# Kernel optimization log

Measured on AMD Instinct MI355X. Metric: run time of the kernel, lower is better.

The kernel has to match this reference:

```python
import jax, jax.numpy as jnp
import numpy as np

K = 16          # hardcoded in generate_graph (self.k = 16, KNNGraph(k=16))
TEMP = 0.5      # gumbel-softmax temperature
GRID = 0.5      # grid_size init arg
EPS = 1e-20


def mlp2(h, W1, b1, W2, b2):
    # tgnn.models.MLP(num_layers=2): Linear -> BN(eval init = identity) -> ReLU -> Linear
    return jax.nn.relu(h @ W1 + b1) @ W2 + b2


def pairwise_sqdist(a, b):
    d2 = (a * a).sum(-1)[:, None] + (b * b).sum(-1)[None, :] - 2.0 * (a @ b.T)
    return jnp.maximum(d2, 0.0)


def setup_inputs() -> dict:
    key = jax.random.key(0)
    ks = jax.random.split(key, 16)
    N, Cin, Cout = 8192, 64, 128

    def lin(k, fi, fo):
        return jax.random.normal(k, (fi, fo), jnp.float32) / np.sqrt(fi)

    return dict(
        x=jax.random.normal(ks[0], (N, Cin), jnp.float32),
        pos=jax.random.uniform(ks[1], (N, 3), jnp.float32) * 10.0,
        # generate_graph.MLP: Cin -> Cin -> 10
        Wg1=lin(ks[2], Cin, Cin), bg1=jnp.zeros((Cin,), jnp.float32),
        Wg2=lin(ks[3], Cin, 10), bg2=jnp.zeros((10,), jnp.float32),
        # PointTransformerConv linears (bias=False in PyG)
        Wlin=lin(ks[4], Cin, Cout),
        Wsrc=lin(ks[5], Cin, Cout),
        Wdst=lin(ks[6], Cin, Cout),
        # pos_nn MLP: 3 -> Cout -> Cout
        Wp1=lin(ks[7], 3, Cout), bp1=jnp.zeros((Cout,), jnp.float32),
        Wp2=lin(ks[8], Cout, Cout), bp2=jnp.zeros((Cout,), jnp.float32),
        # attn_nn MLP: Cout -> Cout -> Cout
        Wa1=lin(ks[9], Cout, Cout), ba1=jnp.zeros((Cout,), jnp.float32),
        Wa2=lin(ks[10], Cout, Cout), ba2=jnp.zeros((Cout,), jnp.float32),
        # down: Linear -> BN(eval identity) -> ReLU
        Wd=lin(ks[11], Cout, Cout), bd=jnp.zeros((Cout,), jnp.float32),
    )


def forward_core(x, pos, Wg1, bg1, Wg2, bg2, Wlin, Wsrc, Wdst,
                 Wp1, bp1, Wp2, bp2, Wa1, ba1, Wa2, ba2, Wd, bd):
    N = x.shape[0]
    rk = jax.random.split(jax.random.key(42), 2)

    # ---- KNNGraph(k=16) on pos: sources = k nearest neighbors, targets = centers ----
    d2p = pairwise_sqdist(pos, pos)
    d2p = d2p.at[jnp.arange(N), jnp.arange(N)].set(jnp.inf)
    _, knn_idx = jax.lax.top_k(-d2p, K)              # [N, K]
    tgt = jnp.repeat(jnp.arange(N), K)               # [N*K]
    knn_src = knn_idx.reshape(-1)

    # ---- gumbel-softmax soft edges on learned embedding ----
    emb = mlp2(x, Wg1, bg1, Wg2, bg2)                # [N, 10]
    emb = emb + jax.random.uniform(rk[0], emb.shape, emb.dtype) * 0.001
    d2e = pairwise_sqdist(emb, emb)                  # dist**2, [N, N]
    u = jax.random.uniform(rk[1], (N, N), jnp.float32)
    gumbel = -jnp.log(-jnp.log(u + EPS) + EPS)
    noisy = jnp.log(jnp.exp(-d2e) + EPS) + gumbel
    probs = jax.nn.softmax(noisy / TEMP, axis=0)     # softmax over dim 0, as in source
    top_v, top_i = jax.lax.top_k(probs, K)           # topk over last axis
    soft_src = top_i.reshape(-1)

    # combined edge_index = [soft edges ; knn edges]  (generate_graph cat order)
    src = jnp.concatenate([soft_src, knn_src])
    dst = jnp.concatenate([tgt, tgt])
    w = jnp.concatenate([top_v.reshape(-1), jnp.ones((N * K,), x.dtype)])

    # ---- PointTransformerConv (vector attention); soft edges weighted by gumbel probs ----
    a_src = (x @ Wsrc)[src]                          # [E, C]
    a_dst = (x @ Wdst)[dst]
    v_src = (x @ Wlin)[src]
    delta = mlp2(pos[dst] - pos[src], Wp1, bp1, Wp2, bp2)     # [E, C]
    logits = mlp2(a_dst - a_src + delta, Wa1, ba1, Wa2, ba2)  # [E, C]
    m = jax.ops.segment_max(logits, dst, num_segments=N)
    e = jnp.exp(logits - m[dst])
    s = jax.ops.segment_sum(e, dst, num_segments=N)
    attn = e / (s[dst] + 1e-16)                      # per-target softmax
    msg = attn * (v_src + delta) * w[:, None]
    h = jax.ops.segment_sum(msg, dst, num_segments=N)         # [N, C]

    # ---- down: Linear -> BN(eval, identity at init) -> ReLU ----
    h = jax.nn.relu(h @ Wd + bd)

    # ---- max_pool_neighbor_x (max over neighbors incl. self-loop) ----
    pooled = jax.ops.segment_max(h[src], dst, num_segments=N)
    h = jnp.maximum(h, pooled)

    # ---- GridSampling(GRID): mean-pool x and pos per voxel, padded to N clusters ----
    v = jnp.floor((pos - pos.min(axis=0)) / GRID).astype(jnp.int32)
    nv = v.max(axis=0) + 1
    vid = (v[:, 0] * nv[1] + v[:, 1]) * nv[2] + v[:, 2]
    _, inv = jnp.unique(vid, size=N, fill_value=-1, return_inverse=True)
    cnt = jax.ops.segment_sum(jnp.ones((N,), x.dtype), inv, num_segments=N)
    denom = jnp.maximum(cnt, 1.0)[:, None]
    x_out = jax.ops.segment_sum(h, inv, num_segments=N) / denom
    pos_out = jax.ops.segment_sum(pos, inv, num_segments=N) / denom
    return x_out, pos_out, cnt


def reference(x, pos, Wg1, bg1, Wg2, bg2, Wlin, Wsrc, Wdst,
              Wp1, bp1, Wp2, bp2, Wa1, ba1, Wa2, ba2, Wd, bd):
    return forward_core(x, pos, Wg1, bg1, Wg2, bg2, Wlin, Wsrc, Wdst,
                        Wp1, bp1, Wp2, bp2, Wa1, ba1, Wa2, ba2, Wd, bd)
```

## Files before the change

### kernel.cpp

```cpp
#include <hip/hip_runtime.h>
#include <stdint.h>


typedef unsigned int u32;
typedef float v2f __attribute__((ext_vector_type(2)));
typedef float f32x4 __attribute__((ext_vector_type(4)));
typedef short bf16x8 __attribute__((ext_vector_type(8)));

#define NN 8192
#define EPS20 1e-20f
#define QSCALE 489.0671f

__host__ __device__ static inline u32 bf16rne(float x){
  u32 b = __float_as_uint(x);
  return (b + 0x7fffu + ((b>>16)&1u)) >> 16;
}

__host__ __device__ static inline u32 rotl32(u32 v, int r){ return (v<<r)|(v>>(32-r)); }

__host__ __device__ static inline void tf2x32(u32 k0, u32 k1, u32 c0, u32 c1, u32& o0, u32& o1){
  u32 ks2 = k0 ^ k1 ^ 0x1BD11BDAu;
  u32 x0 = c0 + k0;
  u32 x1 = c1 + k1;
#define TFR(r) x0 += x1; x1 = rotl32(x1,(r)); x1 ^= x0;
  TFR(13) TFR(15) TFR(26) TFR(6)
  x0 += k1;  x1 += ks2 + 1u;
  TFR(17) TFR(29) TFR(16) TFR(24)
  x0 += ks2; x1 += k0 + 2u;
  TFR(13) TFR(15) TFR(26) TFR(6)
  x0 += k0;  x1 += k1 + 3u;
  TFR(17) TFR(29) TFR(16) TFR(24)
  x0 += k1;  x1 += ks2 + 4u;
  TFR(13) TFR(15) TFR(26) TFR(6)
  x0 += ks2; x1 += k0 + 5u;
#undef TFR
  o0 = x0; o1 = x1;
}

__device__ static inline u32 rbits(u32 k0, u32 k1, u32 idx){
  u32 o0,o1; tf2x32(k0,k1, 0u, idx, o0,o1);
  return o0 ^ o1;
}

__device__ static inline float u01(u32 b){
  return __uint_as_float((b>>9) | 0x3f800000u) - 1.0f;
}

__device__ static inline float gumbel_g(u32 ub){
  float u = u01(ub);
  float w = -__logf(u + EPS20);
  return -__logf(w + EPS20);
}

static constexpr size_t OFF_EMBF = 0;
static constexpr size_t OFF_SP   = OFF_EMBF + (size_t)8192*12*4;
static constexpr size_t OFF_PSUM = OFF_SP   + (size_t)8192*4;
static constexpr size_t OFF_SSRC = OFF_PSUM + (size_t)32*8192*4;
static constexpr size_t OFF_TOPV = OFF_SSRC + (size_t)8192*16*4;
static constexpr size_t OFF_KSRC = OFF_TOPV + (size_t)8192*16*4;
static constexpr size_t OFF_HIST = OFF_KSRC + (size_t)8192*16*4;
static constexpr size_t OFF_RANK = OFF_HIST + (size_t)8192*4;
static constexpr size_t OFF_UCNT = OFF_RANK + (size_t)8192*4;
static constexpr size_t OFF_VID  = OFF_UCNT + (size_t)8192*4;
static constexpr size_t OFF_META = OFF_VID  + (size_t)8192*4;
static constexpr size_t OFF_QKI  = OFF_META + 64;
static constexpr size_t OFF_CAND = OFF_QKI  + (size_t)8192*4;
static constexpr size_t OFF_POS4 = OFF_CAND + (size_t)8192*32*4;
static constexpr size_t OFF_WH   = (OFF_POS4 + (size_t)8192*16 + 255) & ~(size_t)255;
static constexpr size_t OFF_WL   = OFF_WH + (size_t)3*16384*2;
static constexpr size_t OFF_BIG  = (OFF_WL + (size_t)3*16384*2 + 255) & ~(size_t)255;
static constexpr size_t OFF_A    = OFF_BIG;
static constexpr size_t OFF_B    = OFF_A    + (size_t)8192*128*4;
static constexpr size_t OFF_V    = OFF_B    + (size_t)8192*128*4;
static constexpr size_t OFF_H    = OFF_V    + (size_t)8192*128*4;
static constexpr size_t OFF_HD   = OFF_H    + (size_t)8192*128*4;
static constexpr size_t OFF_Y    = OFF_HD   + (size_t)8192*128*4;
static constexpr size_t OFF_ACCX = OFF_Y    + (size_t)8192*128*4;
static constexpr size_t OFF_ACCP = OFF_ACCX + (size_t)8192*128*4;
static constexpr size_t OFF_ZQ   = OFF_BIG;
static constexpr size_t ZQ_BYTES = (size_t)NN*NN*2;


__global__ void k_init0(int* __restrict__ mi, int* __restrict__ mx){
  int t = threadIdx.x;
  if (t < 3){ mi[t] = 0x7f7fffff; mx[t] = 0; }
}

__global__ __launch_bounds__(128) void k_wprep(const float* __restrict__ Wp2,
    const float* __restrict__ Wa1, const float* __restrict__ Wa2,
    unsigned short* __restrict__ WH, unsigned short* __restrict__ WL){
  int m = blockIdx.x >> 7;
  int c = blockIdx.x & 127;
  int k = threadIdx.x;
  const float* Wm = (m==0) ? Wp2 : (m==1) ? Wa1 : Wa2;
  float x = Wm[k*128 + c];
  u32 hi = bf16rne(x);
  float lo = x - __uint_as_float(hi<<16);
  u32 lo16 = bf16rne(lo);
  size_t base = (size_t)m*16384 + (size_t)c*128 + k;
  WH[base] = (unsigned short)hi;
  WL[base] = (unsigned short)lo16;
}

__global__ __launch_bounds__(256) void k_min(const float* __restrict__ pos, int* __restrict__ mi){
  __shared__ int red[768];
  int t = threadIdx.x;
  int n = blockIdx.x*256 + t;
  red[t]     = __float_as_int(pos[n*3+0]);
  red[256+t] = __float_as_int(pos[n*3+1]);
  red[512+t] = __float_as_int(pos[n*3+2]);
  __syncthreads();
  for (int s=128; s>0; s>>=1){
    if (t < s){
      red[t]     = min(red[t],     red[t+s]);
      red[256+t] = min(red[256+t], red[256+t+s]);
      red[512+t] = min(red[512+t], red[512+t+s]);
    }
    __syncthreads();
  }
  if (t == 0){ atomicMin(&mi[0], red[0]); atomicMin(&mi[1], red[256]); atomicMin(&mi[2], red[512]); }
}

__global__ __launch_bounds__(256) void k_ext(const float* __restrict__ pos, const int* __restrict__ mi,
                                             int* __restrict__ mx){
  __shared__ int red[768];
  int t = threadIdx.x;
  int n = blockIdx.x*256 + t;
  float p0 = __int_as_float(mi[0]), p1 = __int_as_float(mi[1]), p2 = __int_as_float(mi[2]);
  red[t]     = (int)floorf((pos[n*3+0]-p0)*2.0f);
  red[256+t] = (int)floorf((pos[n*3+1]-p1)*2.0f);
  red[512+t] = (int)floorf((pos[n*3+2]-p2)*2.0f);
  __syncthreads();
  for (int s=128; s>0; s>>=1){
    if (t < s){
      red[t]     = max(red[t],     red[t+s]);
      red[256+t] = max(red[256+t], red[256+t+s]);
      red[512+t] = max(red[512+t], red[512+t+s]);
    }
    __syncthreads();
  }
  if (t == 0){ atomicMax(&mx[0], red[0]); atomicMax(&mx[1], red[256]); atomicMax(&mx[2], red[512]); }
}

__global__ __launch_bounds__(256) void k_vid(const float* __restrict__ pos,
                                             const int* __restrict__ mi, const int* __restrict__ mx,
                                             int* __restrict__ vid, int* __restrict__ hist,
                                             float4* __restrict__ pos4){
  int n = blockIdx.x*256 + threadIdx.x;
  float p0=pos[n*3], p1=pos[n*3+1], p2=pos[n*3+2];
  float4 p4; p4.x=p0; p4.y=p1; p4.z=p2; p4.w = p0*p0 + p1*p1 + p2*p2;
  pos4[n] = p4;
  float q0 = __int_as_float(mi[0]), q1 = __int_as_float(mi[1]), q2 = __int_as_float(mi[2]);
  int v0 = (int)floorf((p0-q0)*2.0f);
  int v1 = (int)floorf((p1-q1)*2.0f);
  int v2 = (int)floorf((p2-q2)*2.0f);
  int nv1 = mx[1]+1, nv2 = mx[2]+1;
  int id = (v0*nv1 + v1)*nv2 + v2;
  vid[n] = id;
  atomicAdd(&hist[id], 1);
}

__global__ __launch_bounds__(64) void k_emb(const float* __restrict__ x,
    const float* __restrict__ Wg1, const float* __restrict__ bg1,
    const float* __restrict__ Wg2, const float* __restrict__ bg2,
    u32 ka, u32 kb, float* __restrict__ embF){
  int i = blockIdx.x; int t = threadIdx.x;
  __shared__ float xs[64], hs[64], esq[10];
  xs[t] = x[i*64+t];
  __syncthreads();
  float a = bg1[t];
  for (int k=0; k<64; k++) a += xs[k]*Wg1[k*64+t];
  hs[t] = fmaxf(a, 0.0f);
  __syncthreads();
  if (t < 10){
    float e = bg2[t];
    for (int k=0; k<64; k++) e += hs[k]*Wg2[k*10+t];
    e += u01(rbits(ka, kb, (u32)(i*10+t))) * 0.001f;
    embF[i*12+t] = e;
    esq[t] = e*e;
  }
  __syncthreads();
  if (t == 0){
    float ssum = 0.0f;
    #pragma unroll
    for (int d=0; d<10; d++) ssum += esq[d];
    embF[i*12+10] = ssum;
    embF[i*12+11] = 0.0f;
  }
}

__global__ __launch_bounds__(64) void k_knn(const float4* __restrict__ pos4,
                                            int* __restrict__ knn_src){
  int i = blockIdx.x; int l = threadIdx.x;
  float4 pi = pos4[i];
  float lv[8]; int lj[8];
  #pragma unroll
  for (int s=0; s<8; s++){ lv[s]=1e30f; lj[s]=0x7fffffff; }
  for (int tt=0; tt<128; tt++){
    int j = l + 64*tt;
    float4 pj = pos4[j];
    float d = pi.w + pj.w - 2.0f*(pi.x*pj.x + pi.y*pj.y + pi.z*pj.z);
    d = fmaxf(d, 0.0f);
    if (j != i && d < lv[7]){
      lv[7]=d; lj[7]=j;
      #pragma unroll
      for (int s=7; s>0; s--){
        if (lv[s] < lv[s-1]){ float tv=lv[s]; lv[s]=lv[s-1]; lv[s-1]=tv; int tj=lj[s]; lj[s]=lj[s-1]; lj[s-1]=tj; }
      }
    }
  }
  for (int r=0; r<16; r++){
    float bv = lv[0]; int bj = lj[0];
    #pragma unroll
    for (int off=32; off>=1; off>>=1){
      float ov = __shfl_xor(bv, off);
      int   oj = __shfl_xor(bj, off);
      if (ov < bv || (ov == bv && oj < bj)){ bv = ov; bj = oj; }
    }
    if (l == 0) knn_src[i*16+r] = bj;
    if (lj[0] == bj){
      #pragma unroll
      for (int s=0; s<7; s++){ lv[s]=lv[s+1]; lj[s]=lj[s+1]; }
      lv[7]=1e30f; lj[7]=0x7fffffff;
    }
  }
}

template<bool STZ>
__global__ __launch_bounds__(256) void k_colstats(const float* __restrict__ embF,
                                                  u32 ka, u32 kb, float* __restrict__ psum,
                                                  unsigned short* __restrict__ zq){
  __shared__ float4 sE4[768];
  int t = threadIdx.x;
  int j = blockIdx.x*256 + t;
  int i0 = blockIdx.y*256;
  const float4* gF = (const float4*)embF;
  #pragma unroll
  for (int q=0; q<3; q++) sE4[t + 256*q] = gF[(size_t)i0*3 + t + 256*q];
  __syncthreads();
  float4 b0 = gF[j*3+0], b1 = gF[j*3+1], b2 = gF[j*3+2];
  float sej = b2.z;
  float s = 0.0f;
  unsigned short* zp = STZ ? (zq + ((size_t)i0<<13) + j) : nullptr;
  for (int r=0; r<256; r++){
    float4 a0 = sE4[r*3+0], a1 = sE4[r*3+1], a2 = sE4[r*3+2];
    float dot = a0.x*b0.x + a0.y*b0.y + a0.z*b0.z + a0.w*b0.w
              + a1.x*b1.x + a1.y*b1.y + a1.z*b1.z + a1.w*b1.w
              + a2.x*b2.x + a2.y*b2.y;
    float d2 = fmaxf(a2.z + sej - 2.0f*dot, 0.0f);
    float g = gumbel_g(rbits(ka, kb, (u32)(i0+r)*8192u + (u32)j));
    float z = 2.0f*(g - d2);
    s += __expf(z - 40.0f);
    if (STZ){
      float qf = (z + 100.0f)*QSCALE + 0.5f;
      qf = fminf(fmaxf(qf, 0.0f), 65535.0f);
      *zp = (unsigned short)qf;
      zp += NN;
    }
  }
  psum[blockIdx.y*NN + j] = s;
}

__global__ __launch_bounds__(256) void k_colfin(const float* __restrict__ psum, float* __restrict__ embF,
                                                int* __restrict__ qKi){
  int j = blockIdx.x*256 + threadIdx.x;
  float S = 0.0f;
  for (int c=0; c<32; c++) S += psum[c*NN + j];
  float K = 40.0f + __logf(S);
  embF[j*12+11] = K;
  qKi[j] = (int)((K + 100.0f)*QSCALE + 0.5f);
}

__global__ __launch_bounds__(64) void k_rowtopk(const float* __restrict__ embF,
    u32 ka, u32 kb, int* __restrict__ soft_src, float* __restrict__ top_v){
  int i = blockIdx.x; int l = threadIdx.x;
  const float4* gF = (const float4*)embF;
  float4 b0 = gF[i*3+0], b1 = gF[i*3+1], b2 = gF[i*3+2];
  float sei = b2.z;
  float lv[16]; int lj[16];
  #pragma unroll
  for (int s=0; s<16; s++){ lv[s]=-1e30f; lj[s]=0x7fffffff; }
  for (int tt=0; tt<128; tt++){
    int j = l + 64*tt;
    float4 a0 = gF[j*3+0], a1 = gF[j*3+1], a2 = gF[j*3+2];
    float dot = a0.x*b0.x + a0.y*b0.y + a0.z*b0.z + a0.w*b0.w
              + a1.x*b1.x + a1.y*b1.y + a1.z*b1.z + a1.w*b1.w
              + a2.x*b2.x + a2.y*b2.y;
    float d2 = fmaxf(a2.z + sei - 2.0f*dot, 0.0f);
    float g = gumbel_g(rbits(ka, kb, (u32)i*8192u + (u32)j));
    float z = 2.0f*(g - d2);
    float y = z - a2.w;
    if (y > lv[15]){
      lv[15]=y; lj[15]=j;
      #pragma unroll
      for (int s=15; s>0; s--){
        if (lv[s] > lv[s-1]){ float tv=lv[s]; lv[s]=lv[s-1]; lv[s-1]=tv; int tj=lj[s]; lj[s]=lj[s-1]; lj[s-1]=tj; }
      }
    }
  }
  for (int r=0; r<16; r++){
    float bv = lv[0]; int bj = lj[0];
    #pragma unroll
    for (int off=32; off>=1; off>>=1){
      float ov = __shfl_xor(bv, off);
      int   oj = __shfl_xor(bj, off);
      if (ov > bv || (ov == bv && oj < bj)){ bv = ov; bj = oj; }
    }
    if (l == 0){ soft_src[i*16+r] = bj; top_v[i*16+r] = __expf(bv); }
    if (lj[0] == bj){
      #pragma unroll
      for (int s=0; s<15; s++){ lv[s]=lv[s+1]; lj[s]=lj[s+1]; }
      lv[15]=-1e30f; lj[15]=0x7fffffff;
    }
  }
}

__global__ __launch_bounds__(64) void k_qtopk(const unsigned short* __restrict__ zq,
    const int* __restrict__ qKi, int* __restrict__ cand){
  int i = blockIdx.x; int l = threadIdx.x;
  const uint4* zrow = (const uint4*)(zq + ((size_t)i<<13));
  int lv[8]; int lj[8];
  #pragma unroll
  for (int s=0; s<8; s++){ lv[s]=-0x40000000; lj[s]=0x7fffffff; }
  for (int tt=0; tt<16; tt++){
    int blk = l + 64*tt;
    uint4 zv = zrow[blk];
    int jb = blk*8;
    const int4* qk4 = (const int4*)(qKi + jb);
    int4 ka4 = qk4[0], kb4 = qk4[1];
    u32 wv[4] = {zv.x, zv.y, zv.z, zv.w};
    int qk[8] = {ka4.x,ka4.y,ka4.z,ka4.w, kb4.x,kb4.y,kb4.z,kb4.w};
    #pragma unroll
    for (int c=0; c<8; c++){
      int qz = (int)((wv[c>>1] >> ((c&1)*16)) & 0xffffu);
      int qy = qz - qk[c];
      if (qy > lv[7]){
        lv[7]=qy; lj[7]=jb+c;
        #pragma unroll
        for (int s=7; s>0; s--){
          if (lv[s] > lv[s-1]){ int tv=lv[s]; lv[s]=lv[s-1]; lv[s-1]=tv; int tj=lj[s]; lj[s]=lj[s-1]; lj[s-1]=tj; }
        }
      }
    }
  }
  for (int r=0; r<32; r++){
    int bv = lv[0]; int bj = lj[0];
    #pragma unroll
    for (int off=32; off>=1; off>>=1){
      int ov = __shfl_xor(bv, off);
      int oj = __shfl_xor(bj, off);
      if (ov > bv || (ov == bv && oj < bj)){ bv = ov; bj = oj; }
    }
    if (l == 0) cand[i*32+r] = bj;
    if (lj[0] == bj){
      #pragma unroll
      for (int s=0; s<7; s++){ lv[s]=lv[s+1]; lj[s]=lj[s+1]; }
      lv[7]=-0x40000000; lj[7]=0x7fffffff;
    }
  }
}

__global__ __launch_bounds__(64) void k_rescore(const float* __restrict__ embF,
    const int* __restrict__ cand, u32 ka, u32 kb,
    int* __restrict__ soft_src, float* __restrict__ top_v){
  int i = blockIdx.x; int l = threadIdx.x;
  const float4* gF = (const float4*)embF;
  float4 b0 = gF[i*3+0], b1 = gF[i*3+1], b2 = gF[i*3+2];
  float sei = b2.z;
  float y = -1e30f; int jc = 0x7fffffff;
  if (l < 32){
    jc = cand[i*32+l];
    float4 a0 = gF[jc*3+0], a1 = gF[jc*3+1], a2 = gF[jc*3+2];
    float dot = a0.x*b0.x + a0.y*b0.y + a0.z*b0.z + a0.w*b0.w
              + a1.x*b1.x + a1.y*b1.y + a1.z*b1.z + a1.w*b1.w
              + a2.x*b2.x + a2.y*b2.y;
    float d2 = fmaxf(a2.z + sei - 2.0f*dot, 0.0f);
    float g = gumbel_g(rbits(ka, kb, (u32)i*8192u + (u32)jc));
    float z = 2.0f*(g - d2);
    y = z - a2.w;
  }
  for (int r=0; r<16; r++){
    float bv = y; int bj = jc;
    #pragma unroll
    for (int off=32; off>=1; off>>=1){
      float ov = __shfl_xor(bv, off);
      int   oj = __shfl_xor(bj, off);
      if (ov > bv || (ov == bv && oj < bj)){ bv = ov; bj = oj; }
    }
    if (l == 0){ soft_src[i*16+r] = bj; top_v[i*16+r] = __expf(bv); }
    if (jc == bj){ y = -1e30f; jc = 0x7fffffff; }
  }
}

__global__ __launch_bounds__(128) void k_xw(const float* __restrict__ x,
    const float* __restrict__ Wsrc, const float* __restrict__ Wdst, const float* __restrict__ Wlin,
    float* __restrict__ A, float* __restrict__ B, float* __restrict__ V){
  int g0 = blockIdx.x*8; int c = threadIdx.x;
  __shared__ float xs[8][64];
  for (int idx=c; idx<512; idx+=128) xs[idx>>6][idx&63] = x[(g0 + (idx>>6))*64 + (idx&63)];
  __syncthreads();
  float aA[8], aB[8], aV[8];
  #pragma unroll
  for (int g=0; g<8; g++){ aA[g]=0.0f; aB[g]=0.0f; aV[g]=0.0f; }
  for (int k=0; k<64; k++){
    float ws=Wsrc[k*128+c], wd=Wdst[k*128+c], wl=Wlin[k*128+c];
    #pragma unroll
    for (int g=0; g<8; g++){
      float xv = xs[g][k];
      aA[g] += xv*ws; aB[g] += xv*wd; aV[g] += xv*wl;
    }
  }
  #pragma unroll
  for (int g=0; g<8; g++){
    A[(g0+g)*128+c]=aA[g]; B[(g0+g)*128+c]=aB[g]; V[(g0+g)*128+c]=aV[g];
  }
}

#define MFMA3(WHP, WLP)                                                     \
  {                                                                         \
    _Pragma("unroll")                                                       \
    for (int s=0; s<4; s++){                                                \
      int kk = 32*s + 8*g;                                                  \
      bf16x8 a0h = *(const bf16x8*)(&ah[r0][kk]);                           \
      bf16x8 a1h = *(const bf16x8*)(&ah[16+r0][kk]);                        \
      bf16x8 a0l = *(const bf16x8*)(&al[r0][kk]);                           \
      bf16x8 a1l = *(const bf16x8*)(&al[16+r0][kk]);                        \
      const unsigned short* whp = (WHP) + (size_t)cn0*128 + kk;             \
      const unsigned short* wlp = (WLP) + (size_t)cn0*128 + kk;             \
      bf16x8 b0h = *(const bf16x8*)(whp);                                   \
      bf16x8 b1h = *(const bf16x8*)(whp + 2048);                            \
      bf16x8 b0l = *(const bf16x8*)(wlp);                                   \
      bf16x8 b1l = *(const bf16x8*)(wlp + 2048);                            \
      c00 = __builtin_amdgcn_mfma_f32_16x16x32_bf16(a0h,b0h,c00,0,0,0);     \
      c01 = __builtin_amdgcn_mfma_f32_16x16x32_bf16(a0h,b1h,c01,0,0,0);     \
      c10 = __builtin_amdgcn_mfma_f32_16x16x32_bf16(a1h,b0h,c10,0,0,0);     \
      c11 = __builtin_amdgcn_mfma_f32_16x16x32_bf16(a1h,b1h,c11,0,0,0);     \
      c00 = __builtin_amdgcn_mfma_f32_16x16x32_bf16(a0h,b0l,c00,0,0,0);     \
      c01 = __builtin_amdgcn_mfma_f32_16x16x32_bf16(a0h,b1l,c01,0,0,0);     \
      c10 = __builtin_amdgcn_mfma_f32_16x16x32_bf16(a1h,b0l,c10,0,0,0);     \
      c11 = __builtin_amdgcn_mfma_f32_16x16x32_bf16(a1h,b1l,c11,0,0,0);     \
      c00 = __builtin_amdgcn_mfma_f32_16x16x32_bf16(a0l,b0h,c00,0,0,0);     \
      c01 = __builtin_amdgcn_mfma_f32_16x16x32_bf16(a0l,b1h,c01,0,0,0);     \
      c10 = __builtin_amdgcn_mfma_f32_16x16x32_bf16(a1l,b0h,c10,0,0,0);     \
      c11 = __builtin_amdgcn_mfma_f32_16x16x32_bf16(a1l,b1h,c11,0,0,0);     \
    }                                                                       \
  }

__global__ __launch_bounds__(256) void k_edge(const float* __restrict__ pos,
    const int* __restrict__ soft_src, const float* __restrict__ top_v, const int* __restrict__ knn_src,
    const float* __restrict__ A, const float* __restrict__ B, const float* __restrict__ V,
    const float* __restrict__ Wp1, const float* __restrict__ bp1,
    const unsigned short* __restrict__ WH, const unsigned short* __restrict__ WL,
    const float* __restrict__ bp2, const float* __restrict__ ba1, const float* __restrict__ ba2,
    float* __restrict__ h){
  int i = blockIdx.x; int t = threadIdx.x;
  int l = t & 63; int w = t >> 6;
  int g = l >> 4; int r0 = l & 15;
  int cn0 = 32*w + r0;
  __shared__ __align__(16) unsigned short ah[32][136];
  __shared__ __align__(16) unsigned short al[32][136];
  __shared__ int   ssrc[32];
  __shared__ float sw[32];
  __shared__ float sdp[32][3];
  if (t < 32){
    int s; float wt;
    if (t < 16){ s = soft_src[i*16+t]; wt = top_v[i*16+t]; }
    else       { s = knn_src[i*16+(t-16)]; wt = 1.0f; }
    ssrc[t]=s; sw[t]=wt;
    sdp[t][0]=pos[i*3]-pos[s*3]; sdp[t][1]=pos[i*3+1]-pos[s*3+1]; sdp[t][2]=pos[i*3+2]-pos[s*3+2];
  }
  __syncthreads();
  {
    const float2* W1v = (const float2*)Wp1;
    float2 q0 = W1v[l], q1 = W1v[64+l], q2 = W1v[128+l];
    float2 bb = ((const float2*)bp1)[l];
    #pragma unroll
    for (int e=0; e<8; e++){
      int row = 8*w + e;
      float d0=sdp[row][0], d1=sdp[row][1], d2=sdp[row][2];
      float vx = fmaxf(d0*q0.x + d1*q1.x + d2*q2.x + bb.x, 0.0f);
      float vy = fmaxf(d0*q0.y + d1*q1.y + d2*q2.y + bb.y, 0.0f);
      u32 hx = bf16rne(vx), hy = bf16rne(vy);
      float lx = vx - __uint_as_float(hx<<16);
      float ly = vy - __uint_as_float(hy<<16);
      u32 lx16 = bf16rne(lx), ly16 = bf16rne(ly);
      *(u32*)(&ah[row][2*l]) = hx | (hy<<16);
      *(u32*)(&al[row][2*l]) = lx16 | (ly16<<16);
    }
  }
  __syncthreads();
  f32x4 c00={0,0,0,0}, c01={0,0,0,0}, c10={0,0,0,0}, c11={0,0,0,0};
  MFMA3(WH, WL);
  f32x4 dl00, dl01, dl10, dl11;
  {
    float bi0 = bp2[cn0], bi1 = bp2[cn0+16];
    #pragma unroll
    for (int r=0; r<4; r++){
      dl00[r]=c00[r]+bi0; dl01[r]=c01[r]+bi1;
      dl10[r]=c10[r]+bi0; dl11[r]=c11[r]+bi1;
    }
  }
  __syncthreads();
  int ssv[8];
  {
    float B0 = B[(size_t)i*128 + cn0];
    float B1 = B[(size_t)i*128 + cn0 + 16];
    #pragma unroll
    for (int m=0; m<2; m++){
      #pragma unroll
      for (int r=0; r<4; r++){
        int row = 16*m + 4*g + r;
        int sv = ssrc[row]; ssv[m*4+r] = sv;
        float a0 = A[(size_t)sv*128 + cn0];
        float a1 = A[(size_t)sv*128 + cn0 + 16];
        float q0 = B0 - a0 + (m ? dl10[r] : dl00[r]);
        float q1 = B1 - a1 + (m ? dl11[r] : dl01[r]);
        u32 h0 = bf16rne(q0); float lf0 = q0 - __uint_as_float(h0<<16);
        u32 h1 = bf16rne(q1); float lf1 = q1 - __uint_as_float(h1<<16);
        ah[row][cn0]    = (unsigned short)h0;  al[row][cn0]    = (unsigned short)bf16rne(lf0);
        ah[row][cn0+16] = (unsigned short)h1;  al[row][cn0+16] = (unsigned short)bf16rne(lf1);
      }
    }
  }
  __syncthreads();
  c00=(f32x4){0,0,0,0}; c01=c00; c10=c00; c11=c00;
  MFMA3(WH + 16384, WL + 16384);
  __syncthreads();
  {
    float b0v = ba1[cn0], b1v = ba1[cn0+16];
    #pragma unroll
    for (int m=0; m<2; m++){
      #pragma unroll
      for (int r=0; r<4; r++){
        int row = 16*m + 4*g + r;
        float v0 = fmaxf((m ? c10[r] : c00[r]) + b0v, 0.0f);
        float v1 = fmaxf((m ? c11[r] : c01[r]) + b1v, 0.0f);
        u32 h0 = bf16rne(v0); float lf0 = v0 - __uint_as_float(h0<<16);
        u32 h1 = bf16rne(v1); float lf1 = v1 - __uint_as_float(h1<<16);
        ah[row][cn0]    = (unsigned short)h0;  al[row][cn0]    = (unsigned short)bf16rne(lf0);
        ah[row][cn0+16] = (unsigned short)h1;  al[row][cn0+16] = (unsigned short)bf16rne(lf1);
      }
    }
  }
  __syncthreads();
  c00=(f32x4){0,0,0,0}; c01=c00; c10=c00; c11=c00;
  MFMA3(WH + 32768, WL + 32768);
  {
    float b0v = ba2[cn0], b1v = ba2[cn0+16];
    float lg[2][2][4];
    float M0 = -1e30f, M1 = -1e30f;
    #pragma unroll
    for (int m=0; m<2; m++){
      #pragma unroll
      for (int r=0; r<4; r++){
        lg[m][0][r] = (m ? c10[r] : c00[r]) + b0v;
        lg[m][1][r] = (m ? c11[r] : c01[r]) + b1v;
        M0 = fmaxf(M0, lg[m][0][r]);
        M1 = fmaxf(M1, lg[m][1][r]);
      }
    }
    M0 = fmaxf(M0, __shfl_xor(M0, 16)); M0 = fmaxf(M0, __shfl_xor(M0, 32));
    M1 = fmaxf(M1, __shfl_xor(M1, 16)); M1 = fmaxf(M1, __shfl_xor(M1, 32));
    float s0=0.0f, s1=0.0f, o0=0.0f, o1=0.0f;
    #pragma unroll
    for (int m=0; m<2; m++){
      #pragma unroll
      for (int r=0; r<4; r++){
        int row = 16*m + 4*g + r;
        int sv = ssv[m*4+r]; float wt = sw[row];
        float p0 = __expf(lg[m][0][r] - M0);
        float p1 = __expf(lg[m][1][r] - M1);
        s0 += p0; s1 += p1;
        float v0 = V[(size_t)sv*128 + cn0];
        float v1 = V[(size_t)sv*128 + cn0 + 16];
        o0 += p0*(v0 + (m ? dl10[r] : dl00[r]))*wt;
        o1 += p1*(v1 + (m ? dl11[r] : dl01[r]))*wt;
      }
    }
    s0 += __shfl_xor(s0, 16); s0 += __shfl_xor(s0, 32);
    s1 += __shfl_xor(s1, 16); s1 += __shfl_xor(s1, 32);
    o0 += __shfl_xor(o0, 16); o0 += __shfl_xor(o0, 32);
    o1 += __shfl_xor(o1, 16); o1 += __shfl_xor(o1, 32);
    if (g == 0){
      h[(size_t)i*128 + cn0]      = o0/(s0 + 1e-16f);
      h[(size_t)i*128 + cn0 + 16] = o1/(s1 + 1e-16f);
    }
  }
}

__global__ __launch_bounds__(128) void k_down(const float* __restrict__ h,
    const float* __restrict__ Wd, const float* __restrict__ bd, float* __restrict__ hd){
  int g0 = blockIdx.x*8; int c = threadIdx.x;
  __shared__ float hs[8][128];
  for (int idx=c; idx<1024; idx+=128) hs[idx>>7][idx&127] = h[(g0 + (idx>>7))*128 + (idx&127)];
  __syncthreads();
  float acc[8]; float b = bd[c];
  #pragma unroll
  for (int g=0; g<8; g++) acc[g] = b;
  for (int k=0; k<128; k+=4){
    float w0=Wd[(k+0)*128+c], w1=Wd[(k+1)*128+c], w2=Wd[(k+2)*128+c], w3=Wd[(k+3)*128+c];
    #pragma unroll
    for (int g=0; g<8; g++){
      const float4 ev = *(const float4*)(&hs[g][k]);
      acc[g] += ev.x*w0 + ev.y*w1 + ev.z*w2 + ev.w*w3;
    }
  }
  #pragma unroll
  for (int g=0; g<8; g++) hd[(g0+g)*128+c] = fmaxf(acc[g], 0.0f);
}

__global__ __launch_bounds__(128) void k_pool(const float* __restrict__ hd,
    const int* __restrict__ soft_src, const int* __restrict__ knn_src, float* __restrict__ y){
  int i = blockIdx.x; int c = threadIdx.x;
  __shared__ int ss[32];
  if (c < 16) ss[c] = soft_src[i*16+c];
  else if (c < 32) ss[c] = knn_src[i*16+(c-16)];
  __syncthreads();
  float p = hd[i*128+c];
  for (int e=0; e<32; e++) p = fmaxf(p, hd[ss[e]*128+c]);
  y[i*128+c] = p;
}

__global__ __launch_bounds__(256) void k_scan(const int* __restrict__ hist,
    int* __restrict__ rank, int* __restrict__ ucnt, int* __restrict__ Uo){
  __shared__ int part[256];
  int t = threadIdx.x;
  int base = t*32;
  int cnt = 0;
  for (int b=0; b<32; b++) cnt += (hist[base+b] > 0);
  part[t] = cnt;
  __syncthreads();
  if (t == 0){
    int run = 0;
    for (int q=0; q<256; q++){ int v = part[q]; part[q] = run; run += v; }
    Uo[0] = run;
  }
  __syncthreads();
  int run = part[t];
  for (int b=0; b<32; b++){
    int bin = base + b;
    rank[bin] = run;
    int hv = hist[bin];
    if (hv > 0){ ucnt[run] = hv; run++; }
  }
}

__global__ __launch_bounds__(128) void k_agg(const float* __restrict__ y, const float* __restrict__ pos,
    const int* __restrict__ vid, const int* __restrict__ rank,
    float* __restrict__ accx, float* __restrict__ accp){
  int n = blockIdx.x; int c = threadIdx.x;
  int r = rank[vid[n]];
  atomicAdd(&accx[r*128+c], y[n*128+c]);
  if (c < 3) atomicAdd(&accp[r*3+c], pos[n*3+c]);
}

__global__ __launch_bounds__(128) void k_final(const float* __restrict__ accx, const float* __restrict__ accp,
    const int* __restrict__ ucnt, const int* __restrict__ Uo, float* __restrict__ out){
  int r = blockIdx.x; int c = threadIdx.x;
  int u = Uo[0];
  float cnt = (r < u) ? (float)ucnt[r] : 0.0f;
  float den = fmaxf(cnt, 1.0f);
  out[r*128+c] = (r < u) ? accx[r*128+c]/den : 0.0f;
  if (c < 3) out[(size_t)NN*128 + r*3 + c] = (r < u) ? accp[r*3+c]/den : 0.0f;
  if (c == 0) out[(size_t)NN*128 + (size_t)NN*3 + r] = cnt;
}

extern "C" void kernel_launch(void* const* d_in, const int* in_sizes, int n_in,
                              void* d_out, int out_size, void* d_ws, size_t ws_size,
                              hipStream_t stream){
  (void)in_sizes; (void)n_in; (void)out_size;
  const float* x    = (const float*)d_in[0];
  const float* pos  = (const float*)d_in[1];
  const float* Wg1  = (const float*)d_in[2];
  const float* bg1  = (const float*)d_in[3];
  const float* Wg2  = (const float*)d_in[4];
  const float* bg2  = (const float*)d_in[5];
  const float* Wlin = (const float*)d_in[6];
  const float* Wsrc = (const float*)d_in[7];
  const float* Wdst = (const float*)d_in[8];
  const float* Wp1  = (const float*)d_in[9];
  const float* bp1  = (const float*)d_in[10];
  const float* Wp2  = (const float*)d_in[11];
  const float* bp2  = (const float*)d_in[12];
  const float* Wa1  = (const float*)d_in[13];
  const float* ba1  = (const float*)d_in[14];
  const float* Wa2  = (const float*)d_in[15];
  const float* ba2  = (const float*)d_in[16];
  const float* Wd   = (const float*)d_in[17];
  const float* bd   = (const float*)d_in[18];

  char* ws = (char*)d_ws;
  float* embF   = (float*)(ws + OFF_EMBF);
  float* psum   = (float*)(ws + OFF_PSUM);
  int*   ssrc   = (int*)  (ws + OFF_SSRC);
  float* topv   = (float*)(ws + OFF_TOPV);
  int*   ksrc   = (int*)  (ws + OFF_KSRC);
  int*   hist   = (int*)  (ws + OFF_HIST);
  int*   rank   = (int*)  (ws + OFF_RANK);
  int*   ucnt   = (int*)  (ws + OFF_UCNT);
  int*   vid    = (int*)  (ws + OFF_VID);
  int*   mi     = (int*)  (ws + OFF_META);
  int*   mx     = (int*)  (ws + OFF_META + 16);
  int*   Uo     = (int*)  (ws + OFF_META + 32);
  int*   qKi    = (int*)  (ws + OFF_QKI);
  int*   cand   = (int*)  (ws + OFF_CAND);
  float4* pos4  = (float4*)(ws + OFF_POS4);
  unsigned short* WH = (unsigned short*)(ws + OFF_WH);
  unsigned short* WL = (unsigned short*)(ws + OFF_WL);
  float* A      = (float*)(ws + OFF_A);
  float* B      = (float*)(ws + OFF_B);
  float* V      = (float*)(ws + OFF_V);
  float* h      = (float*)(ws + OFF_H);
  float* hd     = (float*)(ws + OFF_HD);
  float* y      = (float*)(ws + OFF_Y);
  float* accx   = (float*)(ws + OFF_ACCX);
  float* accp   = (float*)(ws + OFF_ACCP);
  unsigned short* zq = (unsigned short*)(ws + OFF_ZQ);

  const bool use_q = (ws_size >= OFF_ZQ + ZQ_BYTES);

  u32 rk0a, rk0b, rk1a, rk1b;
  tf2x32(0u, 42u, 0u, 0u, rk0a, rk0b);
  tf2x32(0u, 42u, 0u, 1u, rk1a, rk1b);

  hipMemsetAsync(hist, 0, 8192*4, stream);
  k_wprep<<<384, 128, 0, stream>>>(Wp2, Wa1, Wa2, WH, WL);
  k_init0<<<1, 64, 0, stream>>>(mi, mx);
  k_min<<<32, 256, 0, stream>>>(pos, mi);
  k_ext<<<32, 256, 0, stream>>>(pos, mi, mx);
  k_vid<<<32, 256, 0, stream>>>(pos, mi, mx, vid, hist, pos4);
  k_emb<<<8192, 64, 0, stream>>>(x, Wg1, bg1, Wg2, bg2, rk0a, rk0b, embF);
  k_knn<<<8192, 64, 0, stream>>>(pos4, ksrc);
  if (use_q){
    k_colstats<true><<<dim3(32,32), 256, 0, stream>>>(embF, rk1a, rk1b, psum, zq);
    k_colfin<<<32, 256, 0, stream>>>(psum, embF, qKi);
    k_qtopk<<<8192, 64, 0, stream>>>(zq, qKi, cand);
    k_rescore<<<8192, 64, 0, stream>>>(embF, cand, rk1a, rk1b, ssrc, topv);
  } else {
    k_colstats<false><<<dim3(32,32), 256, 0, stream>>>(embF, rk1a, rk1b, psum, nullptr);
    k_colfin<<<32, 256, 0, stream>>>(psum, embF, qKi);
    k_rowtopk<<<8192, 64, 0, stream>>>(embF, rk1a, rk1b, ssrc, topv);
  }
  k_xw<<<1024, 128, 0, stream>>>(x, Wsrc, Wdst, Wlin, A, B, V);
  k_edge<<<8192, 256, 0, stream>>>(pos, ssrc, topv, ksrc, A, B, V,
                                   Wp1, bp1, WH, WL, bp2, ba1, ba2, h);
  k_down<<<1024, 128, 0, stream>>>(h, Wd, bd, hd);
  k_pool<<<8192, 128, 0, stream>>>(hd, ssrc, ksrc, y);
  hipMemsetAsync(accx, 0, (size_t)8192*128*4, stream);
  hipMemsetAsync(accp, 0, (size_t)8192*3*4, stream);
  k_scan<<<1, 256, 0, stream>>>(hist, rank, ucnt, Uo);
  k_agg<<<8192, 128, 0, stream>>>(y, pos, vid, rank, accx, accp);
  k_final<<<8192, 128, 0, stream>>>(accx, accp, ucnt, Uo, (float*)d_out);
}
```

Baseline: 797.2 us.

## Fuse rescore into quantized top-k, prefetch edge gathers, unroll colstats loop

Merges k_rescore into k_qtopk: candidates stay in registers (lane r keeps candidate r) instead of being written to and reread from a global buffer, which removes one launch per pipeline. In k_edge, the gathers of A, B and V rows are issued before the MFMA phases so their latency can overlap the matrix work. k_colstats gets an incremental RNG counter, unroll by 4 and a rotate builtin to trim per-iteration integer work. The prefetches raise register pressure in k_edge, which may lower occupancy.

```diff
diff --git a/kernel.cpp b/kernel.cpp
--- a/kernel.cpp
+++ b/kernel.cpp
@@ -3,7 +3,6 @@
 
 
 typedef unsigned int u32;
-typedef float v2f __attribute__((ext_vector_type(2)));
 typedef float f32x4 __attribute__((ext_vector_type(4)));
 typedef short bf16x8 __attribute__((ext_vector_type(8)));
 
@@ -16,7 +15,7 @@
   return (b + 0x7fffu + ((b>>16)&1u)) >> 16;
 }
 
-__host__ __device__ static inline u32 rotl32(u32 v, int r){ return (v<<r)|(v>>(32-r)); }
+__host__ __device__ static inline u32 rotl32(u32 v, int r){ return __builtin_rotateleft32(v, (u32)r); }
 
 __host__ __device__ static inline void tf2x32(u32 k0, u32 k1, u32 c0, u32 c1, u32& o0, u32& o1){
   u32 ks2 = k0 ^ k1 ^ 0x1BD11BDAu;
@@ -242,13 +241,15 @@
   float sej = b2.z;
   float s = 0.0f;
   unsigned short* zp = STZ ? (zq + ((size_t)i0<<13) + j) : nullptr;
+  u32 idx = (u32)i0*8192u + (u32)j;
+  #pragma unroll 4
   for (int r=0; r<256; r++){
     float4 a0 = sE4[r*3+0], a1 = sE4[r*3+1], a2 = sE4[r*3+2];
     float dot = a0.x*b0.x + a0.y*b0.y + a0.z*b0.z + a0.w*b0.w
               + a1.x*b1.x + a1.y*b1.y + a1.z*b1.z + a1.w*b1.w
               + a2.x*b2.x + a2.y*b2.y;
     float d2 = fmaxf(a2.z + sej - 2.0f*dot, 0.0f);
-    float g = gumbel_g(rbits(ka, kb, (u32)(i0+r)*8192u + (u32)j));
+    float g = gumbel_g(rbits(ka, kb, idx));
     float z = 2.0f*(g - d2);
     s += __expf(z - 40.0f);
     if (STZ){
@@ -257,6 +258,7 @@
       *zp = (unsigned short)qf;
       zp += NN;
     }
+    idx += 8192u;
   }
   psum[blockIdx.y*NN + j] = s;
 }
@@ -316,7 +318,8 @@
 }
 
 __global__ __launch_bounds__(64) void k_qtopk(const unsigned short* __restrict__ zq,
-    const int* __restrict__ qKi, int* __restrict__ cand){
+    const int* __restrict__ qKi, const float* __restrict__ embF,
+    u32 ka, u32 kb, int* __restrict__ soft_src, float* __restrict__ top_v){
   int i = blockIdx.x; int l = threadIdx.x;
   const uint4* zrow = (const uint4*)(zq + ((size_t)i<<13));
   int lv[8]; int lj[8];
@@ -343,6 +346,7 @@
       }
     }
   }
+  int myc = 0x7fffffff;
   for (int r=0; r<32; r++){
     int bv = lv[0]; int bj = lj[0];
     #pragma unroll
@@ -351,25 +355,19 @@
       int oj = __shfl_xor(bj, off);
       if (ov > bv || (ov == bv && oj < bj)){ bv = ov; bj = oj; }
     }
-    if (l == 0) cand[i*32+r] = bj;
+    if (l == r) myc = bj;
     if (lj[0] == bj){
       #pragma unroll
       for (int s=0; s<7; s++){ lv[s]=lv[s+1]; lj[s]=lj[s+1]; }
       lv[7]=-0x40000000; lj[7]=0x7fffffff;
     }
   }
-}
-
-__global__ __launch_bounds__(64) void k_rescore(const float* __restrict__ embF,
-    const int* __restrict__ cand, u32 ka, u32 kb,
-    int* __restrict__ soft_src, float* __restrict__ top_v){
-  int i = blockIdx.x; int l = threadIdx.x;
   const float4* gF = (const float4*)embF;
   float4 b0 = gF[i*3+0], b1 = gF[i*3+1], b2 = gF[i*3+2];
   float sei = b2.z;
   float y = -1e30f; int jc = 0x7fffffff;
-  if (l < 32){
-    jc = cand[i*32+l];
+  if (l < 32 && myc != 0x7fffffff){
+    jc = myc;
     float4 a0 = gF[jc*3+0], a1 = gF[jc*3+1], a2 = gF[jc*3+2];
     float dot = a0.x*b0.x + a0.y*b0.y + a0.z*b0.z + a0.w*b0.w
               + a1.x*b1.x + a1.y*b1.y + a1.z*b1.z + a1.w*b1.w
@@ -488,6 +486,23 @@
       *(u32*)(&al[row][2*l]) = lx16 | (ly16<<16);
     }
   }
+  int ssv[8];
+  float pfA0[8], pfA1[8];
+  float B0, B1;
+  {
+    B0 = B[(size_t)i*128 + cn0];
+    B1 = B[(size_t)i*128 + cn0 + 16];
+    #pragma unroll
+    for (int m=0; m<2; m++){
+      #pragma unroll
+      for (int r=0; r<4; r++){
+        int row = 16*m + 4*g + r;
+        int sv = ssrc[row]; ssv[m*4+r] = sv;
+        pfA0[m*4+r] = A[(size_t)sv*128 + cn0];
+        pfA1[m*4+r] = A[(size_t)sv*128 + cn0 + 16];
+      }
+    }
+  }
   __syncthreads();
   f32x4 c00={0,0,0,0}, c01={0,0,0,0}, c10={0,0,0,0}, c11={0,0,0,0};
   MFMA3(WH, WL);
@@ -501,20 +516,14 @@
     }
   }
   __syncthreads();
-  int ssv[8];
   {
-    float B0 = B[(size_t)i*128 + cn0];
-    float B1 = B[(size_t)i*128 + cn0 + 16];
     #pragma unroll
     for (int m=0; m<2; m++){
       #pragma unroll
       for (int r=0; r<4; r++){
         int row = 16*m + 4*g + r;
-        int sv = ssrc[row]; ssv[m*4+r] = sv;
-        float a0 = A[(size_t)sv*128 + cn0];
-        float a1 = A[(size_t)sv*128 + cn0 + 16];
-        float q0 = B0 - a0 + (m ? dl10[r] : dl00[r]);
-        float q1 = B1 - a1 + (m ? dl11[r] : dl01[r]);
+        float q0 = B0 - pfA0[m*4+r] + (m ? dl10[r] : dl00[r]);
+        float q1 = B1 - pfA1[m*4+r] + (m ? dl11[r] : dl01[r]);
         u32 h0 = bf16rne(q0); float lf0 = q0 - __uint_as_float(h0<<16);
         u32 h1 = bf16rne(q1); float lf1 = q1 - __uint_as_float(h1<<16);
         ah[row][cn0]    = (unsigned short)h0;  al[row][cn0]    = (unsigned short)bf16rne(lf0);
@@ -543,6 +552,16 @@
     }
   }
   __syncthreads();
+  float pfV0[8], pfV1[8];
+  #pragma unroll
+  for (int m=0; m<2; m++){
+    #pragma unroll
+    for (int r=0; r<4; r++){
+      int sv = ssv[m*4+r];
+      pfV0[m*4+r] = V[(size_t)sv*128 + cn0];
+      pfV1[m*4+r] = V[(size_t)sv*128 + cn0 + 16];
+    }
+  }
   c00=(f32x4){0,0,0,0}; c01=c00; c10=c00; c11=c00;
   MFMA3(WH + 32768, WL + 32768);
   {
@@ -567,14 +586,12 @@
       #pragma unroll
       for (int r=0; r<4; r++){
         int row = 16*m + 4*g + r;
-        int sv = ssv[m*4+r]; float wt = sw[row];
+        float wt = sw[row];
         float p0 = __expf(lg[m][0][r] - M0);
         float p1 = __expf(lg[m][1][r] - M1);
         s0 += p0; s1 += p1;
-        float v0 = V[(size_t)sv*128 + cn0];
-        float v1 = V[(size_t)sv*128 + cn0 + 16];
-        o0 += p0*(v0 + (m ? dl10[r] : dl00[r]))*wt;
-        o1 += p1*(v1 + (m ? dl11[r] : dl01[r]))*wt;
+        o0 += p0*(pfV0[m*4+r] + (m ? dl10[r] : dl00[r]))*wt;
+        o1 += p1*(pfV1[m*4+r] + (m ? dl11[r] : dl01[r]))*wt;
       }
     }
     s0 += __shfl_xor(s0, 16); s0 += __shfl_xor(s0, 32);
@@ -703,7 +720,6 @@
   int*   mx     = (int*)  (ws + OFF_META + 16);
   int*   Uo     = (int*)  (ws + OFF_META + 32);
   int*   qKi    = (int*)  (ws + OFF_QKI);
-  int*   cand   = (int*)  (ws + OFF_CAND);
   float4* pos4  = (float4*)(ws + OFF_POS4);
   unsigned short* WH = (unsigned short*)(ws + OFF_WH);
   unsigned short* WL = (unsigned short*)(ws + OFF_WL);
@@ -734,8 +750,7 @@
   if (use_q){
     k_colstats<true><<<dim3(32,32), 256, 0, stream>>>(embF, rk1a, rk1b, psum, zq);
     k_colfin<<<32, 256, 0, stream>>>(psum, embF, qKi);
-    k_qtopk<<<8192, 64, 0, stream>>>(zq, qKi, cand);
-    k_rescore<<<8192, 64, 0, stream>>>(embF, cand, rk1a, rk1b, ssrc, topv);
+    k_qtopk<<<8192, 64, 0, stream>>>(zq, qKi, embF, rk1a, rk1b, ssrc, topv);
   } else {
     k_colstats<false><<<dim3(32,32), 256, 0, stream>>>(embF, rk1a, rk1b, psum, nullptr);
     k_colfin<<<32, 256, 0, stream>>>(psum, embF, qKi);
```

New measurement: 757.8 us. 1.05x faster.
